# Kernel optimization log

Measured on AMD Instinct MI355X. Metric: run time of the kernel, lower is better.

Reference implementation:

```python
import jax, jax.numpy as jnp
import numpy as np

B, O, F = 64, 64, 1024
RN, RD = 16, 256
DEPTH = 2


def setup_inputs() -> dict:
    key = jax.random.key(0)
    ks = jax.random.split(key, 7)
    s_self = (2.0 / (F + F)) ** 0.5  # xavier-ish scale
    s_rel = (2.0 / (F + RD + F)) ** 0.5
    return {
        "x": jax.random.normal(ks[0], (B, O, F), jnp.float32),
        "A": jax.random.uniform(ks[1], (B, O, O * RN), jnp.float32),
        "R": jax.random.normal(ks[2], (RN, RD), jnp.float32),
        "Wself": jax.random.normal(ks[3], (DEPTH, F, F), jnp.float32) * s_self,
        "bself": jax.random.normal(ks[4], (DEPTH, F), jnp.float32) * 0.02,
        "Wrel": jax.random.normal(ks[5], (DEPTH, F + RD, F), jnp.float32) * s_rel,
        "brel": jax.random.normal(ks[6], (DEPTH, F), jnp.float32) * 0.02,
    }


def reference(x, A, R, Wself, bself, Wrel, brel):
    # x: [B,O,F], A: [B,O,O*RN], R: [RN,RD]
    b, o, f = x.shape
    rn = R.shape[0]
    depth = Wself.shape[0]
    for i in range(depth):
        # self transform: Linear(F -> F)
        xs = x @ Wself[i] + bself[i]  # [B,O,F]
        # relation transform: Linear(F+RD -> F) applied to concat(x_repeated, R_repeated).
        # Exact decomposition of the concat: first F rows of Wrel act on x, rest on R.
        xr_x = x @ Wrel[i][:f]                 # [B,O,F]
        xr_r = R @ Wrel[i][f:] + brel[i]       # [RN,F]
        xr = (xr_x[:, :, None, :] + xr_r[None, None, :, :]).reshape(b, o * rn, f)
        agg = jnp.matmul(A, xr)                # [B,O,F]
        x = jnp.tanh(xs + agg + x)             # residual + tanh
    return x
```

## Files before the change

### kernel.cpp

```cpp
#include <hip/hip_runtime.h>
#include <hip/hip_bf16.h>
#include <math.h>

#define B 64
#define O 64
#define F 1024
#define RN 16
#define RD 256
#define DEPTH 2
#define M (B*O)

typedef __attribute__((ext_vector_type(8))) _Float16 half8;
typedef __attribute__((ext_vector_type(4))) float f32x4;

#define RES_SCALE 2048.0f
#define RES_INV  (1.0f/2048.0f)

__device__ __forceinline__ unsigned short h2u(_Float16 h) {
  union { _Float16 h; unsigned short u; } c; c.h = h; return c.u;
}
__device__ __forceinline__ void split2(float x, unsigned short& h, unsigned short& l) {
  _Float16 hh = (_Float16)x;
  _Float16 ll = (_Float16)((x - (float)hh) * RES_SCALE);
  h = h2u(hh); l = h2u(ll);
}

__device__ __forceinline__ void gload_lds16(const unsigned short* g, void* l) {
  __builtin_amdgcn_global_load_lds(
      (const __attribute__((address_space(1))) unsigned int*)g,
      (__attribute__((address_space(3))) unsigned int*)l, 16, 0, 0);
}

__global__ __launch_bounds__(256) void k_prep(const float* __restrict__ A,
                                              const float* __restrict__ X,
                                              float* __restrict__ A1,
                                              float* __restrict__ A2,
                                              unsigned short* __restrict__ Xh,
                                              unsigned short* __restrict__ Xl) {
  __shared__ float row[O * RN];
  const int t = threadIdx.x;
  if (blockIdx.x < 4096) {
    const int bo = blockIdx.x;
    *reinterpret_cast<float4*>(&row[t * 4]) =
        *reinterpret_cast<const float4*>(&A[(size_t)bo * (O * RN) + t * 4]);
    __syncthreads();
    if (t < O) {
      float s = 0.f;
#pragma unroll
      for (int r = 0; r < RN; ++r) s += row[t * RN + r];
      A1[(size_t)bo * O + t] = s;
    } else if (t < O + RN) {
      const int r = t - O;
      float s = 0.f;
#pragma unroll
      for (int o2 = 0; o2 < O; ++o2) s += row[o2 * RN + r];
      A2[(size_t)bo * RN + r] = s;
    }
  } else {
    const size_t i = ((size_t)(blockIdx.x - 4096) * 256 + t) * 4;
    const float4 v = *reinterpret_cast<const float4*>(&X[i]);
    unsigned short h0, h1, h2, h3, l0, l1, l2, l3;
    split2(v.x, h0, l0); split2(v.y, h1, l1); split2(v.z, h2, l2); split2(v.w, h3, l3);
    uint2 hp, lp;
    hp.x = (unsigned)h0 | ((unsigned)h1 << 16); hp.y = (unsigned)h2 | ((unsigned)h3 << 16);
    lp.x = (unsigned)l0 | ((unsigned)l1 << 16); lp.y = (unsigned)l2 | ((unsigned)l3 << 16);
    *reinterpret_cast<uint2*>(&Xh[i]) = hp;
    *reinterpret_cast<uint2*>(&Xl[i]) = lp;
  }
}

__global__ __launch_bounds__(256) void k_prepW(const float* __restrict__ Wself,
                                               const float* __restrict__ Wrel,
                                               const float* __restrict__ brel,
                                               const float* __restrict__ R,
                                               unsigned short* __restrict__ Wht,
                                               unsigned short* __restrict__ Wlt,
                                               float* __restrict__ xrr) {
  __shared__ float T[32][33];
  const int t = threadIdx.x;
  const int bid = blockIdx.x;
  if (bid < 4096) {
    const int z = bid >> 10;
    const int rem = bid & 1023;
    const int k0 = (rem & 31) * 32, n0 = (rem >> 5) * 32;
    const int layer = z >> 1;
    const int sel = z & 1;
    const float* W = sel ? (Wrel + (size_t)layer * (F + RD) * F)
                         : (Wself + (size_t)layer * F * F);
    const size_t obase = (size_t)layer * 2048 * 1024 + (size_t)(sel ? 1024 : 0) * 1024;
    const int r = t >> 3, c4 = (t & 7) << 2;
    const float4 v = *reinterpret_cast<const float4*>(&W[(size_t)(k0 + r) * 1024 + n0 + c4]);
    T[r][c4] = v.x; T[r][c4 + 1] = v.y; T[r][c4 + 2] = v.z; T[r][c4 + 3] = v.w;
    __syncthreads();
    unsigned short h[4], l[4];
#pragma unroll
    for (int j = 0; j < 4; ++j) split2(T[c4 + j][r], h[j], l[j]);
    uint2 hp, lp;
    hp.x = (unsigned)h[0] | ((unsigned)h[1] << 16); hp.y = (unsigned)h[2] | ((unsigned)h[3] << 16);
    lp.x = (unsigned)l[0] | ((unsigned)l[1] << 16); lp.y = (unsigned)l[2] | ((unsigned)l[3] << 16);
    const size_t o = obase + (size_t)(n0 + r) * 1024 + k0 + c4;
    *reinterpret_cast<uint2*>(&Wht[o]) = hp;
    *reinterpret_cast<uint2*>(&Wlt[o]) = lp;
  } else {
    const int r4 = bid - 4096;
    const int layer = r4 >> 6;
    const int idx = r4 & 63;
    const float* Wr = Wrel + (size_t)layer * (F + RD) * F + (size_t)F * F;
    const float* br = brel + (size_t)layer * F;
    const int r = idx >> 2;
    const int n = ((idx & 3) << 8) + t;
    float s = br[n];
    for (int k = 0; k < RD; ++k) s += R[r * RD + k] * Wr[(size_t)k * F + n];
    xrr[(size_t)layer * RN * F + (size_t)r * F + n] = s;
  }
}

__device__ __forceinline__ void stage_tiles8(const unsigned short* __restrict__ Asrc,
                                             const unsigned short* __restrict__ Bsrc,
                                             int bm, int bn, int k0,
                                             int w, int lane,
                                             char* Al, char* Bl) {
  const int srow = lane >> 3;
  const int sin = (lane & 7) << 4;
#pragma unroll
  for (int i = 0; i < 4; ++i) {
    const int c = (w << 2) + i;
    const int cc = c & 15;
    const int row = (cc << 3) + srow;
    const int inrow = sin ^ ((row & 7) << 4);
    const unsigned short* src = (c < 16) ? Asrc : Bsrc;
    const int rbase = (c < 16) ? bm : bn;
    char* ldst = (c < 16) ? Al : Bl;
    gload_lds16(src + ((size_t)(rbase + row) << 10) + k0 + (inrow >> 1), ldst + (cc << 10));
  }
}

__device__ __forceinline__ void compute_tile8(const char* Al, const char* Bl,
                                              int ar, int br, int kbyte,
                                              f32x4 (&acc)[4][2]) {
#pragma unroll
  for (int kk = 0; kk < 2; ++kk) {
    half8 a[4], b[2];
#pragma unroll
    for (int m = 0; m < 4; ++m) {
      const int row = ar + m * 16;
      const int off = (row << 7) + (((kk << 6) + kbyte) ^ ((row & 7) << 4));
      a[m] = *reinterpret_cast<const half8*>(&Al[off]);
    }
#pragma unroll
    for (int n = 0; n < 2; ++n) {
      const int row = br + n * 16;
      const int off = (row << 7) + (((kk << 6) + kbyte) ^ ((row & 7) << 4));
      b[n] = *reinterpret_cast<const half8*>(&Bl[off]);
    }
#pragma unroll
    for (int m = 0; m < 4; ++m)
#pragma unroll
      for (int n = 0; n < 2; ++n)
        acc[m][n] = __builtin_amdgcn_mfma_f32_16x16x32_f16(a[m], b[n], acc[m][n], 0, 0, 0);
  }
}

__device__ __forceinline__ void gemm_piece8(const unsigned short* __restrict__ Asrc,
                                            const unsigned short* __restrict__ Bsrc,
                                            int bm, int bn, int w, int lane,
                                            int ar, int br, int kbyte,
                                            char* Al0, char* Bl0,
                                            char* Al1, char* Bl1,
                                            f32x4 (&acc)[4][2]) {
  stage_tiles8(Asrc, Bsrc, bm, bn, 0, w, lane, Al0, Bl0);
  __syncthreads();
#pragma unroll
  for (int kt = 0; kt < 16; ++kt) {
    char* Ac = (kt & 1) ? Al1 : Al0;
    char* Bc = (kt & 1) ? Bl1 : Bl0;
    char* An = (kt & 1) ? Al0 : Al1;
    char* Bn = (kt & 1) ? Bl0 : Bl1;
    if (kt + 1 < 16)
      stage_tiles8(Asrc, Bsrc, bm, bn, (kt + 1) << 6, w, lane, An, Bn);
    compute_tile8(Ac, Bc, ar, br, kbyte, acc);
    __syncthreads();
  }
}

__global__ __launch_bounds__(512) void k_gemm_mfma(
    const unsigned short* __restrict__ Xh, const unsigned short* __restrict__ Xl,
    const unsigned short* __restrict__ Wht, const unsigned short* __restrict__ Wlt,
    float* __restrict__ xs, float* __restrict__ xrx, int xs_full) {
  __shared__ __align__(16) char Al0[128 * 128];
  __shared__ __align__(16) char Bl0[128 * 128];
  __shared__ __align__(16) char Al1[128 * 128];
  __shared__ __align__(16) char Bl1[128 * 128];
  const int t = threadIdx.x;
  const int lane = t & 63, w = t >> 6;
  const int bid = blockIdx.x;
  const int half = bid & 1;
  int e = bid >> 1;
  e = (e & 7) * 32 + (e >> 3);
  const int bm = (e & 31) * 128;
  const int bn = (e >> 5) * 128 + (half ? 0 : 1024);
  const int wr = w >> 2, wc = w & 3;
  const bool full = (half == 0) || xs_full;

  f32x4 accM[4][2], accR[4][2];
#pragma unroll
  for (int m = 0; m < 4; ++m)
#pragma unroll
    for (int n = 0; n < 2; ++n) { accM[m][n] = (f32x4)0.f; accR[m][n] = (f32x4)0.f; }

  const int ar = wr * 64 + (lane & 15);
  const int br = wc * 32 + (lane & 15);
  const int kbyte = (lane >> 4) << 4;

  gemm_piece8(Xh, Wht, bm, bn, w, lane, ar, br, kbyte, Al0, Bl0, Al1, Bl1, accM);
  if (full) {
    gemm_piece8(Xh, Wlt, bm, bn, w, lane, ar, br, kbyte, Al0, Bl0, Al1, Bl1, accR);
    gemm_piece8(Xl, Wht, bm, bn, w, lane, ar, br, kbyte, Al0, Bl0, Al1, Bl1, accR);
  }

  float* dst = (bn < 1024) ? xs : xrx;
  const int coff = bn & 1023;
  const int lrow = (lane >> 4) << 2;
  const int lcol = lane & 15;
#pragma unroll
  for (int m = 0; m < 4; ++m)
#pragma unroll
    for (int n = 0; n < 2; ++n) {
      const int gr = bm + wr * 64 + m * 16 + lrow;
      const int gc = coff + wc * 32 + n * 16 + lcol;
#pragma unroll
      for (int i = 0; i < 4; ++i)
        dst[((size_t)(gr + i) << 10) + gc] = accM[m][n][i] + accR[m][n][i] * RES_INV;
    }
}

__global__ __launch_bounds__(512) void k_gemm_l2(
    const unsigned short* __restrict__ Xh, const unsigned short* __restrict__ Xl,
    const unsigned short* __restrict__ Wht, const unsigned short* __restrict__ Wlt,
    float* __restrict__ xs, float* __restrict__ xrx,
    float* __restrict__ P1, float* __restrict__ P2) {
  __shared__ __align__(16) char Al0[128 * 128];
  __shared__ __align__(16) char Bl0[128 * 128];
  __shared__ __align__(16) char Al1[128 * 128];
  __shared__ __align__(16) char Bl1[128 * 128];
  const int t = threadIdx.x;
  const int lane = t & 63, w = t >> 6;
  const int bid = blockIdx.x;
  const int role = bid & 3;
  int e = bid >> 2;
  e = (e & 7) * 32 + (e >> 3);
  const int bm = (e & 31) * 128;
  const int colblk = (e >> 5) * 128;
  const int bn = (role == 0) ? colblk : 1024 + colblk;
  const unsigned short* Asrc = (role == 3) ? Xl : Xh;
  const unsigned short* Bsrc = (role == 2) ? Wlt : Wht;
  float* dst = (role == 0) ? xs : (role == 1) ? xrx : (role == 2) ? P1 : P2;
  const int wr = w >> 2, wc = w & 3;

  f32x4 acc[4][2];
#pragma unroll
  for (int m = 0; m < 4; ++m)
#pragma unroll
    for (int n = 0; n < 2; ++n) acc[m][n] = (f32x4)0.f;

  const int ar = wr * 64 + (lane & 15);
  const int br = wc * 32 + (lane & 15);
  const int kbyte = (lane >> 4) << 4;

  gemm_piece8(Asrc, Bsrc, bm, bn, w, lane, ar, br, kbyte, Al0, Bl0, Al1, Bl1, acc);

  const int lrow = (lane >> 4) << 2;
  const int lcol = lane & 15;
#pragma unroll
  for (int m = 0; m < 4; ++m)
#pragma unroll
    for (int n = 0; n < 2; ++n) {
      const int gr = bm + wr * 64 + m * 16 + lrow;
      const int gc = colblk + wc * 32 + n * 16 + lcol;
#pragma unroll
      for (int i = 0; i < 4; ++i)
        dst[((size_t)(gr + i) << 10) + gc] = acc[m][n][i];
    }
}

__global__ __launch_bounds__(256) void k_agg(const float* __restrict__ A1,
                                             const float* __restrict__ A2,
                                             const float* __restrict__ xrx,
                                             const float* __restrict__ P1,
                                             const float* __restrict__ P2,
                                             const float* __restrict__ xrr,
                                             const float* __restrict__ xs,
                                             const float* __restrict__ bias,
                                             const float* __restrict__ xin,
                                             float* __restrict__ xout,
                                             unsigned short* __restrict__ XhO,
                                             unsigned short* __restrict__ XlO,
                                             int use_p) {
  __shared__ float A1s[O][O + 1];
  __shared__ float A2s[O][RN + 1];
  __shared__ float Xls[O][132];
  __shared__ float Rls[RN][132];
  const int b = blockIdx.x;
  const int f0 = blockIdx.y * 128;
  const int t = threadIdx.x;

#pragma unroll
  for (int i = 0; i < 4; ++i) {
    const int gi = i * 1024 + t * 4;
    const float4 v = *reinterpret_cast<const float4*>(&A1[(size_t)b * O * O + gi]);
    const int o = gi >> 6, c = gi & 63;
    A1s[o][c] = v.x; A1s[o][c + 1] = v.y; A1s[o][c + 2] = v.z; A1s[o][c + 3] = v.w;
  }
  {
    const int gi = t * 4;
    const float4 v = *reinterpret_cast<const float4*>(&A2[(size_t)b * O * RN + gi]);
    const int o = gi >> 4, c = gi & 15;
    A2s[o][c] = v.x; A2s[o][c + 1] = v.y; A2s[o][c + 2] = v.z; A2s[o][c + 3] = v.w;
  }
#pragma unroll
  for (int i = 0; i < 8; ++i) {
    const int gi = i * 1024 + t * 4;
    const int o2 = gi >> 7, c = gi & 127;
    const size_t pidx = ((size_t)(b * O + o2)) * F + f0 + c;
    float4 v = *reinterpret_cast<const float4*>(&xrx[pidx]);
    if (use_p) {
      const float4 p1 = *reinterpret_cast<const float4*>(&P1[pidx]);
      const float4 p2 = *reinterpret_cast<const float4*>(&P2[pidx]);
      v.x += (p1.x + p2.x) * RES_INV; v.y += (p1.y + p2.y) * RES_INV;
      v.z += (p1.z + p2.z) * RES_INV; v.w += (p1.w + p2.w) * RES_INV;
    }
    Xls[o2][c] = v.x; Xls[o2][c + 1] = v.y; Xls[o2][c + 2] = v.z; Xls[o2][c + 3] = v.w;
  }
#pragma unroll
  for (int i = 0; i < 2; ++i) {
    const int gi = i * 1024 + t * 4;
    const int r = gi >> 7, c = gi & 127;
    const float4 v = *reinterpret_cast<const float4*>(&xrr[(size_t)r * F + f0 + c]);
    Rls[r][c] = v.x; Rls[r][c + 1] = v.y; Rls[r][c + 2] = v.z; Rls[r][c + 3] = v.w;
  }
  __syncthreads();

  const int ob = (t >> 4) << 2;
  const int fc = (t & 15) << 2;
  float acc[4][8];
#pragma unroll
  for (int i = 0; i < 4; ++i)
#pragma unroll
    for (int j = 0; j < 8; ++j) acc[i][j] = 0.f;

#pragma unroll 4
  for (int o2 = 0; o2 < O; ++o2) {
    const float4 xa = *reinterpret_cast<const float4*>(&Xls[o2][fc]);
    const float4 xb = *reinterpret_cast<const float4*>(&Xls[o2][fc + 64]);
#pragma unroll
    for (int io = 0; io < 4; ++io) {
      const float a = A1s[ob + io][o2];
      acc[io][0] += a * xa.x; acc[io][1] += a * xa.y; acc[io][2] += a * xa.z; acc[io][3] += a * xa.w;
      acc[io][4] += a * xb.x; acc[io][5] += a * xb.y; acc[io][6] += a * xb.z; acc[io][7] += a * xb.w;
    }
  }
#pragma unroll
  for (int r = 0; r < RN; ++r) {
    const float4 xa = *reinterpret_cast<const float4*>(&Rls[r][fc]);
    const float4 xb = *reinterpret_cast<const float4*>(&Rls[r][fc + 64]);
#pragma unroll
    for (int io = 0; io < 4; ++io) {
      const float a = A2s[ob + io][r];
      acc[io][0] += a * xa.x; acc[io][1] += a * xa.y; acc[io][2] += a * xa.z; acc[io][3] += a * xa.w;
      acc[io][4] += a * xb.x; acc[io][5] += a * xb.y; acc[io][6] += a * xb.z; acc[io][7] += a * xb.w;
    }
  }

#pragma unroll
  for (int io = 0; io < 4; ++io) {
    const size_t base = ((size_t)(b * O + ob + io)) * F + f0;
#pragma unroll
    for (int seg = 0; seg < 2; ++seg) {
      const size_t idx = base + seg * 64 + fc;
      const float4 s = *reinterpret_cast<const float4*>(&xs[idx]);
      const float4 bv = *reinterpret_cast<const float4*>(&bias[f0 + seg * 64 + fc]);
      const float4 xi = *reinterpret_cast<const float4*>(&xin[idx]);
      float4 o;
      o.x = tanhf(acc[io][seg * 4 + 0] + s.x + bv.x + xi.x);
      o.y = tanhf(acc[io][seg * 4 + 1] + s.y + bv.y + xi.y);
      o.z = tanhf(acc[io][seg * 4 + 2] + s.z + bv.z + xi.z);
      o.w = tanhf(acc[io][seg * 4 + 3] + s.w + bv.w + xi.w);
      *reinterpret_cast<float4*>(&xout[idx]) = o;
      if (XhO) {
        unsigned short h0, h1, h2, h3, l0, l1, l2, l3;
        split2(o.x, h0, l0); split2(o.y, h1, l1); split2(o.z, h2, l2); split2(o.w, h3, l3);
        uint2 hp, lp;
        hp.x = (unsigned)h0 | ((unsigned)h1 << 16); hp.y = (unsigned)h2 | ((unsigned)h3 << 16);
        lp.x = (unsigned)l0 | ((unsigned)l1 << 16); lp.y = (unsigned)l2 | ((unsigned)l3 << 16);
        *reinterpret_cast<uint2*>(&XhO[idx]) = hp;
        *reinterpret_cast<uint2*>(&XlO[idx]) = lp;
      }
    }
  }
}

extern "C" void kernel_launch(void* const* d_in, const int* in_sizes, int n_in,
                              void* d_out, int out_size, void* d_ws, size_t ws_size,
                              hipStream_t stream) {
  const float* x0    = (const float*)d_in[0];
  const float* A     = (const float*)d_in[1];
  const float* R     = (const float*)d_in[2];
  const float* Wself = (const float*)d_in[3];
  const float* bself = (const float*)d_in[4];
  const float* Wrel  = (const float*)d_in[5];
  const float* brel  = (const float*)d_in[6];
  float* out = (float*)d_out;

  float* ws  = (float*)d_ws;
  float* A1  = ws;
  float* A2  = A1 + (size_t)M * O;
  float* xrr = A2 + (size_t)M * RN;
  float* xs  = xrr + (size_t)2 * RN * F;
  float* xrx = xs + (size_t)M * F;
  float* P1  = xrx + (size_t)M * F;
  float* P2  = P1 + (size_t)M * F;
  unsigned short* Xh  = (unsigned short*)(P2 + (size_t)M * F);
  unsigned short* Xl  = Xh + (size_t)M * F;
  unsigned short* Wht = Xl + (size_t)M * F;
  unsigned short* Wlt = Wht + (size_t)2 * 2048 * 1024;

  k_prep<<<8192, 256, 0, stream>>>(A, x0, A1, A2, Xh, Xl);
  k_prepW<<<4096 + 128, 256, 0, stream>>>(Wself, Wrel, brel, R, Wht, Wlt, xrr);

  k_gemm_mfma<<<512, 512, 0, stream>>>(Xh, Xl, Wht, Wlt, xs, xrx, 1);
  k_agg<<<dim3(B, F / 128), 256, 0, stream>>>(A1, A2, xrx, P1, P2,
                                              xrr, xs, bself, x0, out,
                                              Xh, Xl, 0);
  k_gemm_l2<<<1024, 512, 0, stream>>>(Xh, Xl,
                                      Wht + (size_t)2048 * 1024,
                                      Wlt + (size_t)2048 * 1024,
                                      xs, xrx, P1, P2);
  k_agg<<<dim3(B, F / 128), 256, 0, stream>>>(A1, A2, xrx, P1, P2,
                                              xrr + (size_t)RN * F, xs,
                                              bself + (size_t)F, out, out,
                                              nullptr, nullptr, 1);
}
```

Before: 166.1 us.

## Merge prep kernels, store residual-correction products in fp16, raise MFMA priority

Fuses the two preprocessing kernels into one launch with a shared LDS buffer, removing one launch and its tail. The layer-2 GEMM now writes the low-part correction products P1/P2 as fp16 instead of fp32, halving their write and read traffic in the aggregation kernel. It also wraps the MFMA compute section in s_setprio to favour the matrix-issuing waves. Storing the correction terms in fp16 adds a small rounding error to already-scaled residuals.

```diff
diff --git a/kernel.cpp b/kernel.cpp
--- a/kernel.cpp
+++ b/kernel.cpp
@@ -19,6 +19,9 @@
 __device__ __forceinline__ unsigned short h2u(_Float16 h) {
   union { _Float16 h; unsigned short u; } c; c.h = h; return c.u;
 }
+__device__ __forceinline__ float u2f(unsigned short u) {
+  union { _Float16 h; unsigned short u; } c; c.u = u; return (float)c.h;
+}
 __device__ __forceinline__ void split2(float x, unsigned short& h, unsigned short& l) {
   _Float16 hh = (_Float16)x;
   _Float16 ll = (_Float16)((x - (float)hh) * RES_SCALE);
@@ -31,16 +34,25 @@
       (__attribute__((address_space(3))) unsigned int*)l, 16, 0, 0);
 }
 
-__global__ __launch_bounds__(256) void k_prep(const float* __restrict__ A,
-                                              const float* __restrict__ X,
-                                              float* __restrict__ A1,
-                                              float* __restrict__ A2,
-                                              unsigned short* __restrict__ Xh,
-                                              unsigned short* __restrict__ Xl) {
-  __shared__ float row[O * RN];
+__global__ __launch_bounds__(256) void k_prepAll(const float* __restrict__ A,
+                                                 const float* __restrict__ X,
+                                                 const float* __restrict__ Wself,
+                                                 const float* __restrict__ Wrel,
+                                                 const float* __restrict__ brel,
+                                                 const float* __restrict__ R,
+                                                 float* __restrict__ A1,
+                                                 float* __restrict__ A2,
+                                                 unsigned short* __restrict__ Xh,
+                                                 unsigned short* __restrict__ Xl,
+                                                 unsigned short* __restrict__ Wht,
+                                                 unsigned short* __restrict__ Wlt,
+                                                 float* __restrict__ xrr) {
+  __shared__ float shm[32][33];
   const int t = threadIdx.x;
-  if (blockIdx.x < 4096) {
-    const int bo = blockIdx.x;
+  const int bid = blockIdx.x;
+  if (bid < 4096) {
+    float* row = &shm[0][0];
+    const int bo = bid;
     *reinterpret_cast<float4*>(&row[t * 4]) =
         *reinterpret_cast<const float4*>(&A[(size_t)bo * (O * RN) + t * 4]);
     __syncthreads();
@@ -56,8 +68,8 @@
       for (int o2 = 0; o2 < O; ++o2) s += row[o2 * RN + r];
       A2[(size_t)bo * RN + r] = s;
     }
-  } else {
-    const size_t i = ((size_t)(blockIdx.x - 4096) * 256 + t) * 4;
+  } else if (bid < 8192) {
+    const size_t i = ((size_t)(bid - 4096) * 256 + t) * 4;
     const float4 v = *reinterpret_cast<const float4*>(&X[i]);
     unsigned short h0, h1, h2, h3, l0, l1, l2, l3;
     split2(v.x, h0, l0); split2(v.y, h1, l1); split2(v.z, h2, l2); split2(v.w, h3, l3);
@@ -66,22 +78,10 @@
     lp.x = (unsigned)l0 | ((unsigned)l1 << 16); lp.y = (unsigned)l2 | ((unsigned)l3 << 16);
     *reinterpret_cast<uint2*>(&Xh[i]) = hp;
     *reinterpret_cast<uint2*>(&Xl[i]) = lp;
-  }
-}
-
-__global__ __launch_bounds__(256) void k_prepW(const float* __restrict__ Wself,
-                                               const float* __restrict__ Wrel,
-                                               const float* __restrict__ brel,
-                                               const float* __restrict__ R,
-                                               unsigned short* __restrict__ Wht,
-                                               unsigned short* __restrict__ Wlt,
-                                               float* __restrict__ xrr) {
-  __shared__ float T[32][33];
-  const int t = threadIdx.x;
-  const int bid = blockIdx.x;
-  if (bid < 4096) {
-    const int z = bid >> 10;
-    const int rem = bid & 1023;
+  } else if (bid < 12288) {
+    const int wb = bid - 8192;
+    const int z = wb >> 10;
+    const int rem = wb & 1023;
     const int k0 = (rem & 31) * 32, n0 = (rem >> 5) * 32;
     const int layer = z >> 1;
     const int sel = z & 1;
@@ -90,11 +90,11 @@
     const size_t obase = (size_t)layer * 2048 * 1024 + (size_t)(sel ? 1024 : 0) * 1024;
     const int r = t >> 3, c4 = (t & 7) << 2;
     const float4 v = *reinterpret_cast<const float4*>(&W[(size_t)(k0 + r) * 1024 + n0 + c4]);
-    T[r][c4] = v.x; T[r][c4 + 1] = v.y; T[r][c4 + 2] = v.z; T[r][c4 + 3] = v.w;
+    shm[r][c4] = v.x; shm[r][c4 + 1] = v.y; shm[r][c4 + 2] = v.z; shm[r][c4 + 3] = v.w;
     __syncthreads();
     unsigned short h[4], l[4];
 #pragma unroll
-    for (int j = 0; j < 4; ++j) split2(T[c4 + j][r], h[j], l[j]);
+    for (int j = 0; j < 4; ++j) split2(shm[c4 + j][r], h[j], l[j]);
     uint2 hp, lp;
     hp.x = (unsigned)h[0] | ((unsigned)h[1] << 16); hp.y = (unsigned)h[2] | ((unsigned)h[3] << 16);
     lp.x = (unsigned)l[0] | ((unsigned)l[1] << 16); lp.y = (unsigned)l[2] | ((unsigned)l[3] << 16);
@@ -102,7 +102,7 @@
     *reinterpret_cast<uint2*>(&Wht[o]) = hp;
     *reinterpret_cast<uint2*>(&Wlt[o]) = lp;
   } else {
-    const int r4 = bid - 4096;
+    const int r4 = bid - 12288;
     const int layer = r4 >> 6;
     const int idx = r4 & 63;
     const float* Wr = Wrel + (size_t)layer * (F + RD) * F + (size_t)F * F;
@@ -138,6 +138,7 @@
 __device__ __forceinline__ void compute_tile8(const char* Al, const char* Bl,
                                               int ar, int br, int kbyte,
                                               f32x4 (&acc)[4][2]) {
+  __builtin_amdgcn_s_setprio(1);
 #pragma unroll
   for (int kk = 0; kk < 2; ++kk) {
     half8 a[4], b[2];
@@ -159,6 +160,7 @@
       for (int n = 0; n < 2; ++n)
         acc[m][n] = __builtin_amdgcn_mfma_f32_16x16x32_f16(a[m], b[n], acc[m][n], 0, 0, 0);
   }
+  __builtin_amdgcn_s_setprio(0);
 }
 
 __device__ __forceinline__ void gemm_piece8(const unsigned short* __restrict__ Asrc,
@@ -238,7 +240,7 @@
     const unsigned short* __restrict__ Xh, const unsigned short* __restrict__ Xl,
     const unsigned short* __restrict__ Wht, const unsigned short* __restrict__ Wlt,
     float* __restrict__ xs, float* __restrict__ xrx,
-    float* __restrict__ P1, float* __restrict__ P2) {
+    unsigned short* __restrict__ P1h, unsigned short* __restrict__ P2h) {
   __shared__ __align__(16) char Al0[128 * 128];
   __shared__ __align__(16) char Bl0[128 * 128];
   __shared__ __align__(16) char Al1[128 * 128];
@@ -254,7 +256,6 @@
   const int bn = (role == 0) ? colblk : 1024 + colblk;
   const unsigned short* Asrc = (role == 3) ? Xl : Xh;
   const unsigned short* Bsrc = (role == 2) ? Wlt : Wht;
-  float* dst = (role == 0) ? xs : (role == 1) ? xrx : (role == 2) ? P1 : P2;
   const int wr = w >> 2, wc = w & 3;
 
   f32x4 acc[4][2];
@@ -271,23 +272,38 @@
 
   const int lrow = (lane >> 4) << 2;
   const int lcol = lane & 15;
-#pragma unroll
-  for (int m = 0; m < 4; ++m)
-#pragma unroll
-    for (int n = 0; n < 2; ++n) {
-      const int gr = bm + wr * 64 + m * 16 + lrow;
-      const int gc = colblk + wc * 32 + n * 16 + lcol;
-#pragma unroll
-      for (int i = 0; i < 4; ++i)
-        dst[((size_t)(gr + i) << 10) + gc] = acc[m][n][i];
-    }
+  if (role < 2) {
+    float* dst = (role == 0) ? xs : xrx;
+#pragma unroll
+    for (int m = 0; m < 4; ++m)
+#pragma unroll
+      for (int n = 0; n < 2; ++n) {
+        const int gr = bm + wr * 64 + m * 16 + lrow;
+        const int gc = colblk + wc * 32 + n * 16 + lcol;
+#pragma unroll
+        for (int i = 0; i < 4; ++i)
+          dst[((size_t)(gr + i) << 10) + gc] = acc[m][n][i];
+      }
+  } else {
+    unsigned short* dst = (role == 2) ? P1h : P2h;
+#pragma unroll
+    for (int m = 0; m < 4; ++m)
+#pragma unroll
+      for (int n = 0; n < 2; ++n) {
+        const int gr = bm + wr * 64 + m * 16 + lrow;
+        const int gc = colblk + wc * 32 + n * 16 + lcol;
+#pragma unroll
+        for (int i = 0; i < 4; ++i)
+          dst[((size_t)(gr + i) << 10) + gc] = h2u((_Float16)acc[m][n][i]);
+      }
+  }
 }
 
 __global__ __launch_bounds__(256) void k_agg(const float* __restrict__ A1,
                                              const float* __restrict__ A2,
                                              const float* __restrict__ xrx,
-                                             const float* __restrict__ P1,
-                                             const float* __restrict__ P2,
+                                             const unsigned short* __restrict__ P1h,
+                                             const unsigned short* __restrict__ P2h,
                                              const float* __restrict__ xrr,
                                              const float* __restrict__ xs,
                                              const float* __restrict__ bias,
@@ -324,10 +340,12 @@
     const size_t pidx = ((size_t)(b * O + o2)) * F + f0 + c;
     float4 v = *reinterpret_cast<const float4*>(&xrx[pidx]);
     if (use_p) {
-      const float4 p1 = *reinterpret_cast<const float4*>(&P1[pidx]);
-      const float4 p2 = *reinterpret_cast<const float4*>(&P2[pidx]);
-      v.x += (p1.x + p2.x) * RES_INV; v.y += (p1.y + p2.y) * RES_INV;
-      v.z += (p1.z + p2.z) * RES_INV; v.w += (p1.w + p2.w) * RES_INV;
+      const uint2 p1 = *reinterpret_cast<const uint2*>(&P1h[pidx]);
+      const uint2 p2 = *reinterpret_cast<const uint2*>(&P2h[pidx]);
+      v.x += (u2f((unsigned short)(p1.x & 0xffff)) + u2f((unsigned short)(p2.x & 0xffff))) * RES_INV;
+      v.y += (u2f((unsigned short)(p1.x >> 16))    + u2f((unsigned short)(p2.x >> 16)))    * RES_INV;
+      v.z += (u2f((unsigned short)(p1.y & 0xffff)) + u2f((unsigned short)(p2.y & 0xffff))) * RES_INV;
+      v.w += (u2f((unsigned short)(p1.y >> 16))    + u2f((unsigned short)(p2.y >> 16)))    * RES_INV;
     }
     Xls[o2][c] = v.x; Xls[o2][c + 1] = v.y; Xls[o2][c + 2] = v.z; Xls[o2][c + 3] = v.w;
   }
@@ -417,25 +435,25 @@
   float* xrr = A2 + (size_t)M * RN;
   float* xs  = xrr + (size_t)2 * RN * F;
   float* xrx = xs + (size_t)M * F;
-  float* P1  = xrx + (size_t)M * F;
-  float* P2  = P1 + (size_t)M * F;
-  unsigned short* Xh  = (unsigned short*)(P2 + (size_t)M * F);
+  unsigned short* P1h = (unsigned short*)(xrx + (size_t)M * F);
+  unsigned short* P2h = P1h + (size_t)M * F;
+  unsigned short* Xh  = P2h + (size_t)M * F;
   unsigned short* Xl  = Xh + (size_t)M * F;
   unsigned short* Wht = Xl + (size_t)M * F;
   unsigned short* Wlt = Wht + (size_t)2 * 2048 * 1024;
 
-  k_prep<<<8192, 256, 0, stream>>>(A, x0, A1, A2, Xh, Xl);
-  k_prepW<<<4096 + 128, 256, 0, stream>>>(Wself, Wrel, brel, R, Wht, Wlt, xrr);
+  k_prepAll<<<12416, 256, 0, stream>>>(A, x0, Wself, Wrel, brel, R,
+                                       A1, A2, Xh, Xl, Wht, Wlt, xrr);
 
   k_gemm_mfma<<<512, 512, 0, stream>>>(Xh, Xl, Wht, Wlt, xs, xrx, 1);
-  k_agg<<<dim3(B, F / 128), 256, 0, stream>>>(A1, A2, xrx, P1, P2,
+  k_agg<<<dim3(B, F / 128), 256, 0, stream>>>(A1, A2, xrx, P1h, P2h,
                                               xrr, xs, bself, x0, out,
                                               Xh, Xl, 0);
   k_gemm_l2<<<1024, 512, 0, stream>>>(Xh, Xl,
                                       Wht + (size_t)2048 * 1024,
                                       Wlt + (size_t)2048 * 1024,
-                                      xs, xrx, P1, P2);
-  k_agg<<<dim3(B, F / 128), 256, 0, stream>>>(A1, A2, xrx, P1, P2,
+                                      xs, xrx, P1h, P2h);
+  k_agg<<<dim3(B, F / 128), 256, 0, stream>>>(A1, A2, xrx, P1h, P2h,
                                               xrr + (size_t)RN * F, xs,
                                               bself + (size_t)F, out, out,
                                               nullptr, nullptr, 1);
```

Measured after the change: 161.9 us. -2.5%, faster.
